# Optimization experiments

Hardware: AMD Instinct MI355X
Metric: run time of the kernel (lower is better)

Reference implementation:

```python
import jax, jax.numpy as jnp
import numpy as np

B, D, HID = 16384, 1024, 4096
HALF = D // 2


def setup_inputs() -> dict:
    key = jax.random.key(0)
    ks = jax.random.split(key, 9)
    sc_in = 1.0 / np.sqrt(HALF)
    sc_h = 1.0 / np.sqrt(HID)
    return {
        "z": jax.random.normal(ks[0], (B, D), dtype=jnp.float32),
        "W1s": jax.random.uniform(ks[1], (HALF, HID), jnp.float32, -sc_in, sc_in),
        "b1s": jax.random.uniform(ks[2], (HID,), jnp.float32, -sc_in, sc_in),
        "W2s": jax.random.uniform(ks[3], (HID, HALF), jnp.float32, -sc_h, sc_h),
        "b2s": jax.random.uniform(ks[4], (HALF,), jnp.float32, -sc_h, sc_h),
        "W1t": jax.random.uniform(ks[5], (HALF, HID), jnp.float32, -sc_in, sc_in),
        "b1t": jax.random.uniform(ks[6], (HID,), jnp.float32, -sc_in, sc_in),
        "W2t": jax.random.uniform(ks[7], (HID, HALF), jnp.float32, -sc_h, sc_h),
        "b2t": jax.random.uniform(ks[8], (HALF,), jnp.float32, -sc_h, sc_h),
    }


def reference(z, W1s, b1s, W2s, b2s, W1t, b1t, W2t, b2t):
    # mask_even=True: a = even-indexed features, b = odd-indexed features
    a = z[:, 0::2]  # [B, HALF]
    b = z[:, 1::2]  # [B, HALF]
    # two-layer MLPs for s and t (cond=None -> inp = a)
    s = jnp.maximum(a @ W1s + b1s, 0.0) @ W2s + b2s  # [B, HALF]
    t = jnp.maximum(a @ W1t + b1t, 0.0) @ W2t + b2t  # [B, HALF]
    b_out = b * jnp.exp(s) + t
    logdet = s.sum(axis=1)  # [B]
    # scatter back: a -> even slots, b_out -> odd slots (interleave)
    z_out = jnp.stack([a, b_out], axis=-1).reshape(z.shape)
    return z_out, logdet
```

## Files before the change

### kernel.cpp

```cpp
#include <hip/hip_runtime.h>
#include <hip/hip_bf16.h>
#include <cstdint>
#include <cstddef>

#define BROWS  16384
#define DDIM   1024
#define HID_N  4096
#define HALF_K 512
#define LDH    8192

typedef __attribute__((ext_vector_type(8))) short s8v;
typedef __attribute__((ext_vector_type(4))) float f4v;
typedef __attribute__((ext_vector_type(2))) float f2v;

__device__ __forceinline__ void gload16(const void* g, void* l) {
  __builtin_amdgcn_global_load_lds(
      (const __attribute__((address_space(1))) unsigned int*)g,
      (__attribute__((address_space(3))) unsigned int*)l, 16, 0, 0);
}
#define BAR()   asm volatile("s_barrier" ::: "memory")
#define BARS()  asm volatile("s_waitcnt lgkmcnt(0)\n\ts_barrier" ::: "memory")
#define SCHED0() __builtin_amdgcn_sched_barrier(0)

template <int N> __device__ __forceinline__ void vmw() {
  if constexpr (N == 0)       asm volatile("s_waitcnt vmcnt(0)" ::: "memory");
  else if constexpr (N == 4)  asm volatile("s_waitcnt vmcnt(4)" ::: "memory");
  else if constexpr (N == 10) asm volatile("s_waitcnt vmcnt(10)" ::: "memory");
}

__global__ __launch_bounds__(256) void cast_a_kernel(const float* __restrict__ z,
                                                     __hip_bfloat16* __restrict__ a16) {
  const int idx = blockIdx.x * 256 + threadIdx.x;
  const int m  = idx >> 6;
  const int kb = idx & 63;
  const float4* zp = (const float4*)(z + (size_t)m * DDIM + (size_t)kb * 16);
  alignas(16) __hip_bfloat16 t[8];
#pragma unroll
  for (int i = 0; i < 4; ++i) {
    float4 v = zp[i];
    t[2 * i]     = __float2bfloat16(v.x);
    t[2 * i + 1] = __float2bfloat16(v.z);
  }
  *(s8v*)(a16 + (size_t)m * HALF_K + kb * 8) = *(const s8v*)t;
}

__global__ __launch_bounds__(256) void transpose_cast_kernel(const float* __restrict__ W,
                                                             __hip_bfloat16* __restrict__ WT,
                                                             int K, int N) {
  __shared__ float tile[32][33];
  const int n0 = blockIdx.x * 32, k0 = blockIdx.y * 32;
  const int tx = threadIdx.x & 31;
  const int ty = threadIdx.x >> 5;
#pragma unroll
  for (int i = 0; i < 32; i += 8)
    tile[ty + i][tx] = W[(size_t)(k0 + ty + i) * N + n0 + tx];
  __syncthreads();
#pragma unroll
  for (int i = 0; i < 32; i += 8)
    WT[(size_t)(n0 + ty + i) * K + k0 + tx] = __float2bfloat16(tile[tx][ty + i]);
}

__global__ __launch_bounds__(512, 2)
void gemm1_kernel(const __hip_bfloat16* __restrict__ A,
                  const __hip_bfloat16* __restrict__ BT,
                  const float* __restrict__ b1s, const float* __restrict__ b1t,
                  __hip_bfloat16* __restrict__ Hout) {
  __shared__ alignas(16) char smem[131072];
  constexpr int NT = HALF_K / 64;

  const int nwg = gridDim.x;
  const int orig = blockIdx.x;
  const int vid = (orig & 7) * (nwg >> 3) + (orig >> 3);
  const int bx = vid >> 5, by = vid & 31;
  const int m0 = bx * 256, n0 = by * 256;

  const int tid = threadIdx.x;
  const int trow = tid >> 3;
  const int scol = ((tid & 7) * 16) ^ ((trow & 7) << 4);

  const int lane = tid & 63, wid = tid >> 6;
  const int wr = wid >> 2, wc = wid & 3;
  const int lr = lane & 15, lk = lane >> 4;
  const int xo = (lr & 7) << 4;

  int aoff[4][2], boff[2][2];
#pragma unroll
  for (int j = 0; j < 4; ++j)
#pragma unroll
    for (int kk = 0; kk < 2; ++kk)
      aoff[j][kk] = (j * 32 + wr * 16 + lr) * 128 + ((kk * 64 + lk * 16) ^ xo);
#pragma unroll
  for (int nn = 0; nn < 2; ++nn)
#pragma unroll
    for (int kk = 0; kk < 2; ++kk)
      boff[nn][kk] = (nn * 64 + wc * 16 + lr) * 128 + ((kk * 64 + lk * 16) ^ xo);

  f4v acc[8][4] = {};

  auto stage_A = [&](int h, int T) {
#pragma unroll
    for (int l = 0; l < 2; ++l)
      gload16((const char*)A + (size_t)(m0 + h * 128 + l * 64 + trow) * (HALF_K * 2) + (size_t)T * 128 + scol,
              smem + (T & 1) * 65536 + h * 16384 + l * 8192 + tid * 16);
  };
  auto stage_B = [&](int h, int T) {
#pragma unroll
    for (int l = 0; l < 2; ++l)
      gload16((const char*)BT + (size_t)(n0 + h * 128 + l * 64 + trow) * (HALF_K * 2) + (size_t)T * 128 + scol,
              smem + (T & 1) * 65536 + 32768 + h * 16384 + l * 8192 + tid * 16);
  };

  stage_A(0, 0); stage_B(0, 0); stage_A(1, 0); stage_B(1, 0);
  stage_A(0, 1); stage_B(0, 1);
  vmw<4>();
  BAR();

  for (int T = 0; T < NT; ++T) {
    const char* bufp = smem + (T & 1) * 65536;
    s8v af[4][2], b0r[2][2], b1r[2][2];

#pragma unroll
    for (int j = 0; j < 4; ++j) {
      af[j][0] = *(const s8v*)(bufp + aoff[j][0]);
      af[j][1] = *(const s8v*)(bufp + aoff[j][1]);
    }
#pragma unroll
    for (int nn = 0; nn < 2; ++nn) {
      b0r[nn][0] = *(const s8v*)(bufp + 32768 + boff[nn][0]);
      b0r[nn][1] = *(const s8v*)(bufp + 32768 + boff[nn][1]);
    }
    if (T + 1 < NT) stage_B(1, T + 1);
    BAR(); SCHED0();
    __builtin_amdgcn_s_setprio(1);
#pragma unroll
    for (int j = 0; j < 4; ++j)
#pragma unroll
      for (int nn = 0; nn < 2; ++nn)
#pragma unroll
        for (int kk = 0; kk < 2; ++kk)
          acc[j][nn] = __builtin_amdgcn_mfma_f32_16x16x32_bf16(af[j][kk], b0r[nn][kk], acc[j][nn], 0, 0, 0);
    __builtin_amdgcn_s_setprio(0);
    BAR();

#pragma unroll
    for (int nn = 0; nn < 2; ++nn) {
      b1r[nn][0] = *(const s8v*)(bufp + 49152 + boff[nn][0]);
      b1r[nn][1] = *(const s8v*)(bufp + 49152 + boff[nn][1]);
    }
    if (T + 1 < NT) stage_A(1, T + 1);
    BAR(); SCHED0();
    __builtin_amdgcn_s_setprio(1);
#pragma unroll
    for (int j = 0; j < 4; ++j)
#pragma unroll
      for (int nn = 0; nn < 2; ++nn)
#pragma unroll
        for (int kk = 0; kk < 2; ++kk)
          acc[j][2 + nn] = __builtin_amdgcn_mfma_f32_16x16x32_bf16(af[j][kk], b1r[nn][kk], acc[j][2 + nn], 0, 0, 0);
    __builtin_amdgcn_s_setprio(0);
    BAR();

#pragma unroll
    for (int j = 0; j < 4; ++j) {
      af[j][0] = *(const s8v*)(bufp + 16384 + aoff[j][0]);
      af[j][1] = *(const s8v*)(bufp + 16384 + aoff[j][1]);
    }
    if (T + 2 < NT) stage_A(0, T + 2);
    BAR(); SCHED0();
    __builtin_amdgcn_s_setprio(1);
#pragma unroll
    for (int j = 0; j < 4; ++j)
#pragma unroll
      for (int nn = 0; nn < 2; ++nn)
#pragma unroll
        for (int kk = 0; kk < 2; ++kk)
          acc[4 + j][nn] = __builtin_amdgcn_mfma_f32_16x16x32_bf16(af[j][kk], b0r[nn][kk], acc[4 + j][nn], 0, 0, 0);
    __builtin_amdgcn_s_setprio(0);
    BAR();

    if (T + 2 < NT) stage_B(0, T + 2);
    SCHED0();
    __builtin_amdgcn_s_setprio(1);
#pragma unroll
    for (int j = 0; j < 4; ++j)
#pragma unroll
      for (int nn = 0; nn < 2; ++nn)
#pragma unroll
        for (int kk = 0; kk < 2; ++kk)
          acc[4 + j][2 + nn] = __builtin_amdgcn_mfma_f32_16x16x32_bf16(af[j][kk], b1r[nn][kk], acc[4 + j][2 + nn], 0, 0, 0);
    __builtin_amdgcn_s_setprio(0);
    if (T + 2 >= NT) vmw<0>(); else vmw<4>();
    BAR();
  }

  const float* bp = (n0 < HID_N) ? b1s : b1t;
  const int cb0 = n0 & (HID_N - 1);
  float bv[4];
#pragma unroll
  for (int ni = 0; ni < 4; ++ni) bv[ni] = bp[cb0 + ni * 64 + wc * 16 + lr];

#pragma unroll
  for (int mi = 0; mi < 8; ++mi) {
#pragma unroll
    for (int ni = 0; ni < 4; ++ni) {
      const int cb = (ni * 64 + wc * 16 + lr) * 2;
#pragma unroll
      for (int r = 0; r < 4; ++r) {
        const int row = mi * 32 + wr * 16 + lk * 4 + r;
        const int swz = ((row & 7) << 4) ^ (((row >> 3) & 1) << 8);
        float v = fmaxf(acc[mi][ni][r] + bv[ni], 0.0f);
        *(__hip_bfloat16*)(smem + row * 512 + (cb ^ swz)) = __float2bfloat16(v);
      }
    }
  }
  BARS();
#pragma unroll
  for (int i = 0; i < 16; ++i) {
    const int bo = tid * 16 + i * 8192;
    const int row = bo >> 9, cb = bo & 511;
    const int swz = ((row & 7) << 4) ^ (((row >> 3) & 1) << 8);
    s8v v = *(const s8v*)(smem + row * 512 + (cb ^ swz));
    *(s8v*)((char*)Hout + ((size_t)(m0 + row) * LDH + n0) * 2 + cb) = v;
  }
}

__global__ __launch_bounds__(512, 1)
void gemm2_kernel(const __hip_bfloat16* __restrict__ H,
                  const __hip_bfloat16* __restrict__ BsT,
                  const __hip_bfloat16* __restrict__ BtT,
                  const float* __restrict__ b2s, const float* __restrict__ b2t,
                  const float* __restrict__ zin, float* __restrict__ zout,
                  float* __restrict__ gpart) {
  __shared__ alignas(16) char smem[163840];
  constexpr int NT = HID_N / 64;
  constexpr int BUF = 81920;

  const int nwg = gridDim.x;
  const int orig = blockIdx.x;
  const int vid = (orig & 7) * (nwg >> 3) + (orig >> 3);
  const int rb = vid >> 3, by = vid & 7;
  const int m0 = rb * 256, n0c = by * 64;

  const int tid = threadIdx.x;
  const int trow = tid >> 3;
  const int scol = ((tid & 7) * 16) ^ ((trow & 7) << 4);

  const int lane = tid & 63, wid = tid >> 6;
  const int wr = wid >> 1, ws = wid & 1;
  const int lr = lane & 15, lk = lane >> 4;
  const int xo = (lr & 7) << 4;

  int aoff[4][2], boff[4][2];
#pragma unroll
  for (int f = 0; f < 4; ++f)
#pragma unroll
    for (int kk = 0; kk < 2; ++kk) {
      aoff[f][kk] = (wr * 64 + f * 16 + lr) * 128 + ((kk * 64 + lk * 16) ^ xo);
      boff[f][kk] = (f * 16 + lr) * 128 + ((kk * 64 + lk * 16) ^ xo);
    }
  const int aLds = ws * 32768;
  const int bLds = 65536 + ws * 8192;

  f4v acc[4][4] = {};

  auto stage = [&](int T) {
    const size_t tcol = (size_t)T * 128 + scol;
#pragma unroll
    for (int l = 0; l < 4; ++l)
      gload16((const char*)H + (size_t)(m0 + l * 64 + trow) * (LDH * 2) + tcol,
              smem + (T & 1) * BUF + l * 8192 + tid * 16);
#pragma unroll
    for (int l = 0; l < 4; ++l)
      gload16((const char*)H + (size_t)(m0 + l * 64 + trow) * (LDH * 2) + 8192 + tcol,
              smem + (T & 1) * BUF + 32768 + l * 8192 + tid * 16);
    gload16((const char*)BsT + (size_t)(n0c + trow) * (HID_N * 2) + tcol,
            smem + (T & 1) * BUF + 65536 + tid * 16);
    gload16((const char*)BtT + (size_t)(n0c + trow) * (HID_N * 2) + tcol,
            smem + (T & 1) * BUF + 73728 + tid * 16);
  };

  stage(0); stage(1);
  vmw<10>();
  BAR();

  for (int T = 0; T < NT; ++T) {
    const char* bufp = smem + (T & 1) * BUF;
    s8v af[4][2], bf[4][2];
#pragma unroll
    for (int f = 0; f < 4; ++f) {
      af[f][0] = *(const s8v*)(bufp + aLds + aoff[f][0]);
      af[f][1] = *(const s8v*)(bufp + aLds + aoff[f][1]);
    }
#pragma unroll
    for (int f = 0; f < 4; ++f) {
      bf[f][0] = *(const s8v*)(bufp + bLds + boff[f][0]);
      bf[f][1] = *(const s8v*)(bufp + bLds + boff[f][1]);
    }
    __builtin_amdgcn_s_setprio(1);
#pragma unroll
    for (int fm = 0; fm < 4; ++fm)
#pragma unroll
      for (int fn = 0; fn < 4; ++fn)
#pragma unroll
        for (int kk = 0; kk < 2; ++kk)
          acc[fm][fn] = __builtin_amdgcn_mfma_f32_16x16x32_bf16(af[fm][kk], bf[fn][kk], acc[fm][fn], 0, 0, 0);
    __builtin_amdgcn_s_setprio(0);
    BAR();
    if (T + 2 < NT) { stage(T + 2); vmw<10>(); }
    else if (T + 1 < NT) { vmw<0>(); }
    BAR();
  }

  const float* bp2 = ws ? b2t : b2s;
  float bv[4];
#pragma unroll
  for (int fn = 0; fn < 4; ++fn) bv[fn] = bp2[n0c + fn * 16 + lr];

  float* slds = (float*)smem;
  if (ws == 0) {
#pragma unroll
    for (int fm = 0; fm < 4; ++fm)
#pragma unroll
      for (int fn = 0; fn < 4; ++fn)
#pragma unroll
        for (int r = 0; r < 4; ++r) {
          const int row = wr * 64 + fm * 16 + lk * 4 + r;
          slds[row * 68 + fn * 16 + lr] = acc[fm][fn][r] + bv[fn];
        }
  }
  BARS();
  if (ws == 1) {
    float pl[4][4] = {};
#pragma unroll
    for (int fm = 0; fm < 4; ++fm) {
#pragma unroll
      for (int fn = 0; fn < 4; ++fn) {
#pragma unroll
        for (int r = 0; r < 4; ++r) {
          const int row = wr * 64 + fm * 16 + lk * 4 + r;
          const int rr = m0 + row;
          const int cg = n0c + fn * 16 + lr;
          const float sv = slds[row * 68 + fn * 16 + lr];
          const float tv = acc[fm][fn][r] + bv[fn];
          pl[fm][r] += sv;
          const size_t base = (size_t)rr * DDIM + 2 * cg;
          float2 zv = *(const float2*)(zin + base);
          f2v o;
          o.x = zv.x;
          o.y = zv.y * __expf(sv) + tv;
          __builtin_nontemporal_store(o, (f2v*)(zout + base));
        }
      }
    }
#pragma unroll
    for (int m = 1; m < 16; m <<= 1)
#pragma unroll
      for (int fm = 0; fm < 4; ++fm)
#pragma unroll
        for (int r = 0; r < 4; ++r)
          pl[fm][r] += __shfl_xor(pl[fm][r], m, 64);
    if (lr == 0) {
#pragma unroll
      for (int fm = 0; fm < 4; ++fm)
#pragma unroll
        for (int r = 0; r < 4; ++r) {
          const int rr = m0 + wr * 64 + fm * 16 + lk * 4 + r;
          gpart[(size_t)rr * 8 + by] = pl[fm][r];
        }
    }
  }
}

__global__ __launch_bounds__(256) void ld_reduce_kernel(const float* __restrict__ gpart,
                                                        float* __restrict__ ld) {
  const int r = blockIdx.x * 256 + threadIdx.x;
  const float4* g = (const float4*)(gpart + (size_t)r * 8);
  float4 v0 = g[0], v1 = g[1];
  ld[r] = ((v0.x + v0.y) + (v0.z + v0.w)) + ((v1.x + v1.y) + (v1.z + v1.w));
}

extern "C" void kernel_launch(void* const* d_in, const int* in_sizes, int n_in,
                              void* d_out, int out_size, void* d_ws, size_t ws_size,
                              hipStream_t stream) {
  const float* z   = (const float*)d_in[0];
  const float* W1s = (const float*)d_in[1];
  const float* b1s = (const float*)d_in[2];
  const float* W2s = (const float*)d_in[3];
  const float* b2s = (const float*)d_in[4];
  const float* W1t = (const float*)d_in[5];
  const float* b1t = (const float*)d_in[6];
  const float* W2t = (const float*)d_in[7];
  const float* b2t = (const float*)d_in[8];
  float* zout = (float*)d_out;
  float* ld   = zout + (size_t)BROWS * DDIM;

  char* ws = (char*)d_ws;
  __hip_bfloat16* a16    = (__hip_bfloat16*)ws;
  __hip_bfloat16* w1catT = (__hip_bfloat16*)(ws + 16777216);
  __hip_bfloat16* w2sT   = (__hip_bfloat16*)(ws + 25165824);
  __hip_bfloat16* w2tT   = (__hip_bfloat16*)(ws + 29360128);
  float*          gpart  = (float*)(ws + 33554432);
  char*           hbase  = ws + 34078720;

  int CH = 2048;
  for (int c = 8192; c >= 2048; c >>= 1) {
    if (34078720ull + (size_t)c * 16384ull <= ws_size) { CH = c; break; }
  }
  __hip_bfloat16* H = (__hip_bfloat16*)hbase;

  cast_a_kernel<<<BROWS * (HALF_K / 8) / 256, 256, 0, stream>>>(z, a16);
  transpose_cast_kernel<<<dim3(128, 16), 256, 0, stream>>>(W1s, w1catT, HALF_K, HID_N);
  transpose_cast_kernel<<<dim3(128, 16), 256, 0, stream>>>(W1t, w1catT + (size_t)HID_N * HALF_K, HALF_K, HID_N);
  transpose_cast_kernel<<<dim3(16, 128), 256, 0, stream>>>(W2s, w2sT, HID_N, HALF_K);
  transpose_cast_kernel<<<dim3(16, 128), 256, 0, stream>>>(W2t, w2tT, HID_N, HALF_K);

  for (int mb = 0; mb < BROWS; mb += CH) {
    const int SUB = (CH >= 4096) ? 4096 : CH;
    for (int sub = 0; sub < CH; sub += SUB) {
      gemm1_kernel<<<(SUB / 256) * 32, 512, 0, stream>>>(
          a16 + (size_t)(mb + sub) * HALF_K, w1catT, b1s, b1t,
          H + (size_t)sub * LDH);
    }
    gemm2_kernel<<<(CH / 256) * 8, 512, 0, stream>>>(
        H, w2sT, w2tT, b2s, b2t,
        z + (size_t)mb * DDIM, zout + (size_t)mb * DDIM, gpart + (size_t)mb * 8);
  }
  ld_reduce_kernel<<<BROWS / 256, 256, 0, stream>>>(gpart, ld);
}
```

Measured before the change: 393.6 us.

## Retile gemm2 to 128x128 tiles with two blocks per CU and merge prep kernels

Result: faster. 358.6 us (-8.9%).

```diff
diff --git a/kernel.cpp b/kernel.cpp
--- a/kernel.cpp
+++ b/kernel.cpp
@@ -23,32 +23,16 @@
 #define SCHED0() __builtin_amdgcn_sched_barrier(0)
 
 template <int N> __device__ __forceinline__ void vmw() {
-  if constexpr (N == 0)       asm volatile("s_waitcnt vmcnt(0)" ::: "memory");
-  else if constexpr (N == 4)  asm volatile("s_waitcnt vmcnt(4)" ::: "memory");
-  else if constexpr (N == 10) asm volatile("s_waitcnt vmcnt(10)" ::: "memory");
-}
-
-__global__ __launch_bounds__(256) void cast_a_kernel(const float* __restrict__ z,
-                                                     __hip_bfloat16* __restrict__ a16) {
-  const int idx = blockIdx.x * 256 + threadIdx.x;
-  const int m  = idx >> 6;
-  const int kb = idx & 63;
-  const float4* zp = (const float4*)(z + (size_t)m * DDIM + (size_t)kb * 16);
-  alignas(16) __hip_bfloat16 t[8];
-#pragma unroll
-  for (int i = 0; i < 4; ++i) {
-    float4 v = zp[i];
-    t[2 * i]     = __float2bfloat16(v.x);
-    t[2 * i + 1] = __float2bfloat16(v.z);
-  }
-  *(s8v*)(a16 + (size_t)m * HALF_K + kb * 8) = *(const s8v*)t;
-}
-
-__global__ __launch_bounds__(256) void transpose_cast_kernel(const float* __restrict__ W,
-                                                             __hip_bfloat16* __restrict__ WT,
-                                                             int K, int N) {
+  if constexpr (N == 0)      asm volatile("s_waitcnt vmcnt(0)" ::: "memory");
+  else if constexpr (N == 4) asm volatile("s_waitcnt vmcnt(4)" ::: "memory");
+  else if constexpr (N == 8) asm volatile("s_waitcnt vmcnt(8)" ::: "memory");
+}
+
+__device__ __forceinline__ void transpose_body(const float* __restrict__ W,
+                                               __hip_bfloat16* __restrict__ WT,
+                                               int K, int N, int bx, int by) {
   __shared__ float tile[32][33];
-  const int n0 = blockIdx.x * 32, k0 = blockIdx.y * 32;
+  const int n0 = bx * 32, k0 = by * 32;
   const int tx = threadIdx.x & 31;
   const int ty = threadIdx.x >> 5;
 #pragma unroll
@@ -58,6 +42,44 @@
 #pragma unroll
   for (int i = 0; i < 32; i += 8)
     WT[(size_t)(n0 + ty + i) * K + k0 + tx] = __float2bfloat16(tile[tx][ty + i]);
+}
+
+__global__ __launch_bounds__(256) void prep_kernel(const float* __restrict__ z,
+                                                   __hip_bfloat16* __restrict__ a16,
+                                                   const float* __restrict__ W1s,
+                                                   const float* __restrict__ W1t,
+                                                   const float* __restrict__ W2s,
+                                                   const float* __restrict__ W2t,
+                                                   __hip_bfloat16* __restrict__ w1T,
+                                                   __hip_bfloat16* __restrict__ w2sT,
+                                                   __hip_bfloat16* __restrict__ w2tT) {
+  const int b = blockIdx.x;
+  if (b < 4096) {
+    const int idx = b * 256 + threadIdx.x;
+    const int m  = idx >> 6;
+    const int kb = idx & 63;
+    const float4* zp = (const float4*)(z + (size_t)m * DDIM + (size_t)kb * 16);
+    alignas(16) __hip_bfloat16 t[8];
+#pragma unroll
+    for (int i = 0; i < 4; ++i) {
+      float4 v = zp[i];
+      t[2 * i]     = __float2bfloat16(v.x);
+      t[2 * i + 1] = __float2bfloat16(v.z);
+    }
+    *(s8v*)(a16 + (size_t)m * HALF_K + kb * 8) = *(const s8v*)t;
+  } else if (b < 6144) {
+    const int v = b - 4096;
+    transpose_body(W1s, w1T, HALF_K, HID_N, v & 127, v >> 7);
+  } else if (b < 8192) {
+    const int v = b - 6144;
+    transpose_body(W1t, w1T + (size_t)HID_N * HALF_K, HALF_K, HID_N, v & 127, v >> 7);
+  } else if (b < 10240) {
+    const int v = b - 8192;
+    transpose_body(W2s, w2sT, HID_N, HALF_K, v & 15, v >> 4);
+  } else {
+    const int v = b - 10240;
+    transpose_body(W2t, w2tT, HID_N, HALF_K, v & 15, v >> 4);
+  }
 }
 
 __global__ __launch_bounds__(512, 2)
@@ -224,97 +246,106 @@
   }
 }
 
-__global__ __launch_bounds__(512, 1)
+__global__ __launch_bounds__(512, 2)
 void gemm2_kernel(const __hip_bfloat16* __restrict__ H,
                   const __hip_bfloat16* __restrict__ BsT,
                   const __hip_bfloat16* __restrict__ BtT,
                   const float* __restrict__ b2s, const float* __restrict__ b2t,
                   const float* __restrict__ zin, float* __restrict__ zout,
                   float* __restrict__ gpart) {
-  __shared__ alignas(16) char smem[163840];
+  __shared__ alignas(16) char smem[131072];
   constexpr int NT = HID_N / 64;
-  constexpr int BUF = 81920;
 
   const int nwg = gridDim.x;
   const int orig = blockIdx.x;
   const int vid = (orig & 7) * (nwg >> 3) + (orig >> 3);
-  const int rb = vid >> 3, by = vid & 7;
-  const int m0 = rb * 256, n0c = by * 64;
+  const int rb = vid >> 2, by = vid & 3;
+  const int m0 = rb * 128, n0c = by * 128;
 
   const int tid = threadIdx.x;
   const int trow = tid >> 3;
   const int scol = ((tid & 7) * 16) ^ ((trow & 7) << 4);
 
   const int lane = tid & 63, wid = tid >> 6;
-  const int wr = wid >> 1, ws = wid & 1;
+  const int ws = wid & 1, wc = (wid >> 1) & 1, wr = (wid >> 2) & 1;
   const int lr = lane & 15, lk = lane >> 4;
   const int xo = (lr & 7) << 4;
 
+  const int aBase = ws ? 16384 : 0;
+  const int bBase = ws ? 49152 : 32768;
   int aoff[4][2], boff[4][2];
 #pragma unroll
   for (int f = 0; f < 4; ++f)
 #pragma unroll
     for (int kk = 0; kk < 2; ++kk) {
-      aoff[f][kk] = (wr * 64 + f * 16 + lr) * 128 + ((kk * 64 + lk * 16) ^ xo);
-      boff[f][kk] = (f * 16 + lr) * 128 + ((kk * 64 + lk * 16) ^ xo);
-    }
-  const int aLds = ws * 32768;
-  const int bLds = 65536 + ws * 8192;
+      aoff[f][kk] = aBase + (wr * 64 + f * 16 + lr) * 128 + ((kk * 64 + lk * 16) ^ xo);
+      boff[f][kk] = bBase + (wc * 64 + f * 16 + lr) * 128 + ((kk * 64 + lk * 16) ^ xo);
+    }
 
   f4v acc[4][4] = {};
 
-  auto stage = [&](int T) {
+  auto stage_all = [&](int T) {
+    char* dst = smem + (T & 1) * 65536;
     const size_t tcol = (size_t)T * 128 + scol;
 #pragma unroll
-    for (int l = 0; l < 4; ++l)
+    for (int l = 0; l < 2; ++l)
       gload16((const char*)H + (size_t)(m0 + l * 64 + trow) * (LDH * 2) + tcol,
-              smem + (T & 1) * BUF + l * 8192 + tid * 16);
-#pragma unroll
-    for (int l = 0; l < 4; ++l)
+              dst + l * 8192 + tid * 16);
+#pragma unroll
+    for (int l = 0; l < 2; ++l)
       gload16((const char*)H + (size_t)(m0 + l * 64 + trow) * (LDH * 2) + 8192 + tcol,
-              smem + (T & 1) * BUF + 32768 + l * 8192 + tid * 16);
-    gload16((const char*)BsT + (size_t)(n0c + trow) * (HID_N * 2) + tcol,
-            smem + (T & 1) * BUF + 65536 + tid * 16);
-    gload16((const char*)BtT + (size_t)(n0c + trow) * (HID_N * 2) + tcol,
-            smem + (T & 1) * BUF + 73728 + tid * 16);
+              dst + 16384 + l * 8192 + tid * 16);
+#pragma unroll
+    for (int l = 0; l < 2; ++l)
+      gload16((const char*)BsT + (size_t)(n0c + l * 64 + trow) * (HID_N * 2) + tcol,
+              dst + 32768 + l * 8192 + tid * 16);
+#pragma unroll
+    for (int l = 0; l < 2; ++l)
+      gload16((const char*)BtT + (size_t)(n0c + l * 64 + trow) * (HID_N * 2) + tcol,
+              dst + 49152 + l * 8192 + tid * 16);
   };
 
-  stage(0); stage(1);
-  vmw<10>();
+  stage_all(0);
+  vmw<0>();
   BAR();
 
   for (int T = 0; T < NT; ++T) {
-    const char* bufp = smem + (T & 1) * BUF;
-    s8v af[4][2], bf[4][2];
-#pragma unroll
-    for (int f = 0; f < 4; ++f) {
-      af[f][0] = *(const s8v*)(bufp + aLds + aoff[f][0]);
-      af[f][1] = *(const s8v*)(bufp + aLds + aoff[f][1]);
-    }
-#pragma unroll
-    for (int f = 0; f < 4; ++f) {
-      bf[f][0] = *(const s8v*)(bufp + bLds + boff[f][0]);
-      bf[f][1] = *(const s8v*)(bufp + bLds + boff[f][1]);
-    }
+    const char* bufp = smem + (T & 1) * 65536;
+    s8v af[4], bf[4];
+
+#pragma unroll
+    for (int f = 0; f < 4; ++f) af[f] = *(const s8v*)(bufp + aoff[f][0]);
+#pragma unroll
+    for (int f = 0; f < 4; ++f) bf[f] = *(const s8v*)(bufp + boff[f][0]);
+    if (T + 1 < NT) stage_all(T + 1);
     __builtin_amdgcn_s_setprio(1);
 #pragma unroll
     for (int fm = 0; fm < 4; ++fm)
 #pragma unroll
       for (int fn = 0; fn < 4; ++fn)
-#pragma unroll
-        for (int kk = 0; kk < 2; ++kk)
-          acc[fm][fn] = __builtin_amdgcn_mfma_f32_16x16x32_bf16(af[fm][kk], bf[fn][kk], acc[fm][fn], 0, 0, 0);
-    __builtin_amdgcn_s_setprio(0);
-    BAR();
-    if (T + 2 < NT) { stage(T + 2); vmw<10>(); }
-    else if (T + 1 < NT) { vmw<0>(); }
+        acc[fm][fn] = __builtin_amdgcn_mfma_f32_16x16x32_bf16(af[fm], bf[fn], acc[fm][fn], 0, 0, 0);
+    __builtin_amdgcn_s_setprio(0);
+
+#pragma unroll
+    for (int f = 0; f < 4; ++f) af[f] = *(const s8v*)(bufp + aoff[f][1]);
+#pragma unroll
+    for (int f = 0; f < 4; ++f) bf[f] = *(const s8v*)(bufp + boff[f][1]);
+    __builtin_amdgcn_s_setprio(1);
+#pragma unroll
+    for (int fm = 0; fm < 4; ++fm)
+#pragma unroll
+      for (int fn = 0; fn < 4; ++fn)
+        acc[fm][fn] = __builtin_amdgcn_mfma_f32_16x16x32_bf16(af[fm], bf[fn], acc[fm][fn], 0, 0, 0);
+    __builtin_amdgcn_s_setprio(0);
+
+    if (T + 1 < NT) vmw<0>();
     BAR();
   }
 
   const float* bp2 = ws ? b2t : b2s;
   float bv[4];
 #pragma unroll
-  for (int fn = 0; fn < 4; ++fn) bv[fn] = bp2[n0c + fn * 16 + lr];
+  for (int fn = 0; fn < 4; ++fn) bv[fn] = bp2[n0c + wc * 64 + fn * 16 + lr];
 
   float* slds = (float*)smem;
   if (ws == 0) {
@@ -325,7 +356,8 @@
 #pragma unroll
         for (int r = 0; r < 4; ++r) {
           const int row = wr * 64 + fm * 16 + lk * 4 + r;
-          slds[row * 68 + fn * 16 + lr] = acc[fm][fn][r] + bv[fn];
+          const int col = wc * 64 + fn * 16 + lr;
+          slds[row * 128 + col] = acc[fm][fn][r] + bv[fn];
         }
   }
   BARS();
@@ -338,12 +370,12 @@
 #pragma unroll
         for (int r = 0; r < 4; ++r) {
           const int row = wr * 64 + fm * 16 + lk * 4 + r;
+          const int col = wc * 64 + fn * 16 + lr;
           const int rr = m0 + row;
-          const int cg = n0c + fn * 16 + lr;
-          const float sv = slds[row * 68 + fn * 16 + lr];
+          const float sv = slds[row * 128 + col];
           const float tv = acc[fm][fn][r] + bv[fn];
           pl[fm][r] += sv;
-          const size_t base = (size_t)rr * DDIM + 2 * cg;
+          const size_t base = (size_t)rr * DDIM + 2 * (size_t)(n0c + col);
           float2 zv = *(const float2*)(zin + base);
           f2v o;
           o.x = zv.x;
@@ -365,7 +397,7 @@
 #pragma unroll
         for (int r = 0; r < 4; ++r) {
           const int rr = m0 + wr * 64 + fm * 16 + lk * 4 + r;
-          gpart[(size_t)rr * 8 + by] = pl[fm][r];
+          gpart[(size_t)rr * 8 + by * 2 + wc] = pl[fm][r];
         }
     }
   }
@@ -408,20 +440,17 @@
   }
   __hip_bfloat16* H = (__hip_bfloat16*)hbase;
 
-  cast_a_kernel<<<BROWS * (HALF_K / 8) / 256, 256, 0, stream>>>(z, a16);
-  transpose_cast_kernel<<<dim3(128, 16), 256, 0, stream>>>(W1s, w1catT, HALF_K, HID_N);
-  transpose_cast_kernel<<<dim3(128, 16), 256, 0, stream>>>(W1t, w1catT + (size_t)HID_N * HALF_K, HALF_K, HID_N);
-  transpose_cast_kernel<<<dim3(16, 128), 256, 0, stream>>>(W2s, w2sT, HID_N, HALF_K);
-  transpose_cast_kernel<<<dim3(16, 128), 256, 0, stream>>>(W2t, w2tT, HID_N, HALF_K);
-
+  prep_kernel<<<12288, 256, 0, stream>>>(z, a16, W1s, W1t, W2s, W2t,
+                                         w1catT, w2sT, w2tT);
+
+  const int SUB = (CH >= 4096) ? 4096 : CH;
   for (int mb = 0; mb < BROWS; mb += CH) {
-    const int SUB = (CH >= 4096) ? 4096 : CH;
     for (int sub = 0; sub < CH; sub += SUB) {
       gemm1_kernel<<<(SUB / 256) * 32, 512, 0, stream>>>(
           a16 + (size_t)(mb + sub) * HALF_K, w1catT, b1s, b1t,
           H + (size_t)sub * LDH);
     }
-    gemm2_kernel<<<(CH / 256) * 8, 512, 0, stream>>>(
+    gemm2_kernel<<<(CH / 128) * 4, 512, 0, stream>>>(
         H, w2sT, w2tT, b2s, b2t,
         z + (size_t)mb * DDIM, zout + (size_t)mb * DDIM, gpart + (size_t)mb * 8);
   }
```
